# Kernel optimization log

Measured on AMD Instinct MI355X. Metric: run time of the kernel, lower is better.

## Reference

```python
import jax, jax.numpy as jnp
import numpy as np

N_HEADS = 16

def setup_inputs() -> dict:
    key = jax.random.key(0)
    qkv = jax.random.normal(key, (4, 3072, 1024), dtype=jnp.float32)
    return {"qkv": qkv}

def reference(qkv):
    bs, width, length = qkv.shape
    ch = width // (3 * N_HEADS)
    qkv_h = qkv.reshape(bs * N_HEADS, 3 * ch, length)
    q, k, v = jnp.split(qkv_h, 3, axis=1)  # each [bs*H, ch, T]
    scale = 1.0 / jnp.sqrt(jnp.sqrt(jnp.asarray(ch, qkv.dtype)))
    # [bs*H, T, T] scores
    weight = jnp.einsum('bct,bcs->bts', q * scale, k * scale)
    weight = jax.nn.softmax(weight.astype(jnp.float32), axis=-1).astype(weight.dtype)
    a = jnp.einsum('bts,bcs->bct', weight, v)  # [bs*H, ch, T]
    return a.reshape(bs, -1, length)
```

## Files before the change

### kernel.cpp

```cpp
#include <hip/hip_runtime.h>
#include <hip/hip_bf16.h>


typedef __bf16 bf16_8 __attribute__((ext_vector_type(8)));
typedef __bf16 bf16_4 __attribute__((ext_vector_type(4)));
typedef float floatx4 __attribute__((ext_vector_type(4)));
typedef float floatx16 __attribute__((ext_vector_type(16)));

#define NTHREADS 512
#define STR 64
#define NSTEPS 16

#if __has_builtin(__builtin_amdgcn_exp2f)
#define EXP2(x) __builtin_amdgcn_exp2f(x)
#else
#define EXP2(x) exp2f(x)
#endif
#define QSCALE 0.18033688011112042f

#define LDS_BYTES 57344

#define ZERO16 (floatx16){0.f,0.f,0.f,0.f,0.f,0.f,0.f,0.f,0.f,0.f,0.f,0.f,0.f,0.f,0.f,0.f}

__device__ __forceinline__ int kap(int row) { return ((row >> 1) + (row >> 4)) & 7; }
__device__ __forceinline__ int sigma_row(int s) {
    return (s & 0x33) | ((s & 4) << 1) | ((s & 8) >> 1);
}

__device__ __forceinline__ unsigned pk_bf16(float a, float b) {
    unsigned r;
    asm("v_cvt_pk_bf16_f32 %0, %1, %2" : "=v"(r) : "v"(a), "v"(b));
    return r;
}

union U8 { unsigned u[4]; bf16_8 v; };

__device__ __forceinline__ void write_k(__bf16* kn, const float4* r, int si, int sG) {
    #pragma unroll
    for (int rr = 0; rr < 4; ++rr) {
        int srow = si * 4 + rr;
        int m = sigma_row(srow);
        bf16_4 w;
        w[0] = (__bf16)((const float*)&r[0])[rr];
        w[1] = (__bf16)((const float*)&r[1])[rr];
        w[2] = (__bf16)((const float*)&r[2])[rr];
        w[3] = (__bf16)((const float*)&r[3])[rr];
        *(bf16_4*)&kn[m * STR + ((sG ^ (kap(m) << 1)) << 2)] = w;
    }
}
__device__ __forceinline__ void write_v(__bf16* vn, const float4* r, int si, int c0) {
    #pragma unroll
    for (int jj = 0; jj < 4; ++jj) {
        int c = c0 + jj;
        bf16_4 w;
        w[0] = (__bf16)r[jj].x; w[1] = (__bf16)r[jj].y;
        w[2] = (__bf16)r[jj].z; w[3] = (__bf16)r[jj].w;
        *(bf16_4*)&vn[c * STR + ((si ^ (kap(c) << 1)) << 2)] = w;
    }
}

__global__ __launch_bounds__(NTHREADS, 4)
void attn_kernel(const float* __restrict__ qkv, float* __restrict__ out) {
    __shared__ char smem[LDS_BYTES];
    __bf16* q_s = (__bf16*)smem;
    __bf16* k0  = (__bf16*)(smem + 16384);
    __bf16* k1  = (__bf16*)(smem + 24576);
    __bf16* v0  = (__bf16*)(smem + 32768);
    __bf16* v1  = (__bf16*)(smem + 40960);
    __bf16* v2  = (__bf16*)(smem + 49152);

    const int tid  = threadIdx.x;
    const int wave = tid >> 6;
    const int lane = tid & 63;
    const int hv   = lane >> 5;
    const int l31  = lane & 31;
    const int g    = wave >> 1;
    const int sh   = wave & 1;

    const int bx = blockIdx.x;
    const int bh = bx & 63;
    const int t0 = (bx >> 6) << 7;

    const float* qg = qkv + (size_t)bh * 196608;
    const float* kg = qg + 65536;
    const float* vg = qg + 131072;

    const int sv = tid >> 8;
    const int st = tid & 255;
    const int si = st & 15;
    const int sG = st >> 4;
    const int c0 = sG << 2;
    const float* gsrc = sv ? vg : kg;

    {
        const int cG = tid >> 5;
        const int ti = tid & 31;
        float4 q4[4];
        #pragma unroll
        for (int jj = 0; jj < 4; ++jj)
            q4[jj] = *(const float4*)(qg + (cG * 4 + jj) * 1024 + t0 + ti * 4);
        #pragma unroll
        for (int rr = 0; rr < 4; ++rr) {
            int trow = ti * 4 + rr;
            bf16_4 w;
            w[0] = (__bf16)(((const float*)&q4[0])[rr] * QSCALE);
            w[1] = (__bf16)(((const float*)&q4[1])[rr] * QSCALE);
            w[2] = (__bf16)(((const float*)&q4[2])[rr] * QSCALE);
            w[3] = (__bf16)(((const float*)&q4[3])[rr] * QSCALE);
            *(bf16_4*)&q_s[trow * STR + ((cG ^ (kap(trow) << 1)) << 2)] = w;
        }
    }
    {
        float4 r4[4];
        #pragma unroll
        for (int jj = 0; jj < 4; ++jj)
            r4[jj] = *(const float4*)(gsrc + (c0 + jj) * 1024 + si * 4);
        if (!sv) write_k(k0, r4, si, sG);
        else     write_v(v0, r4, si, c0);
    }
    __syncthreads();

    bf16_8 qf[4];
    {
        int row = g * 32 + l31;
        int x = kap(row);
        #pragma unroll
        for (int kc = 0; kc < 4; ++kc)
            qf[kc] = *(const bf16_8*)&q_s[row * STR + ((((kc << 1) | hv) ^ x) << 3)];
    }

    floatx16 O0 = ZERO16, O1 = ZERO16;
    float l = 0.f;
    bf16_8 pfp0, pfp1;
    int vprev = 2, vcur = 0, vnext = 1;

    const int krow = sh * 32 + l31;
    const int kx   = kap(krow);
    const int vx0  = kap(l31);
    const int vx1  = kap(32 + l31);

    for (int is = 0; is < NSTEPS; ++is) {
        const __bf16* kb = (is & 1) ? k1 : k0;

        float4 pr[4];
        if (is < NSTEPS - 1) {
            const int s0n = (is + 1) * 64;
            #pragma unroll
            for (int jj = 0; jj < 4; ++jj)
                pr[jj] = *(const float4*)(gsrc + (c0 + jj) * 1024 + s0n + si * 4);
        }

        floatx16 St = ZERO16;
        #pragma unroll
        for (int kc = 0; kc < 4; ++kc) {
            bf16_8 kf = *(const bf16_8*)&kb[krow * STR + ((((kc << 1) | hv) ^ kx) << 3)];
            St = __builtin_amdgcn_mfma_f32_32x32x16_bf16(kf, qf[kc], St, 0, 0, 0);
        }

        U8 w0, w1;
        #pragma unroll
        for (int d = 0; d < 4; ++d) {
            float pa = EXP2(St[2 * d]);
            float pb = EXP2(St[2 * d + 1]);
            float pc = EXP2(St[8 + 2 * d]);
            float pd = EXP2(St[8 + 2 * d + 1]);
            l += (pa + pb) + (pc + pd);
            w0.u[d] = pk_bf16(pa, pb);
            w1.u[d] = pk_bf16(pc, pd);
        }
        bf16_8 pfn0 = w0.v, pfn1 = w1.v;

        if (is > 0) {
            const __bf16* vp = (vprev == 0) ? v0 : ((vprev == 1) ? v1 : v2);
            {
                int vrow = l31;
                bf16_8 vfa = *(const bf16_8*)&vp[vrow * STR + ((((sh << 2) | hv) ^ vx0) << 3)];
                O0 = __builtin_amdgcn_mfma_f32_32x32x16_bf16(vfa, pfp0, O0, 0, 0, 0);
                bf16_8 vfb = *(const bf16_8*)&vp[vrow * STR + ((((sh << 2) | 2 | hv) ^ vx0) << 3)];
                O0 = __builtin_amdgcn_mfma_f32_32x32x16_bf16(vfb, pfp1, O0, 0, 0, 0);
            }
            {
                int vrow = 32 + l31;
                bf16_8 vfa = *(const bf16_8*)&vp[vrow * STR + ((((sh << 2) | hv) ^ vx1) << 3)];
                O1 = __builtin_amdgcn_mfma_f32_32x32x16_bf16(vfa, pfp0, O1, 0, 0, 0);
                bf16_8 vfb = *(const bf16_8*)&vp[vrow * STR + ((((sh << 2) | 2 | hv) ^ vx1) << 3)];
                O1 = __builtin_amdgcn_mfma_f32_32x32x16_bf16(vfb, pfp1, O1, 0, 0, 0);
            }
        }
        pfp0 = pfn0; pfp1 = pfn1;

        if (is < NSTEPS - 1) {
            if (!sv) {
                __bf16* kn = (is & 1) ? k0 : k1;
                write_k(kn, pr, si, sG);
            } else {
                __bf16* vn = (vnext == 0) ? v0 : ((vnext == 1) ? v1 : v2);
                write_v(vn, pr, si, c0);
            }
            __syncthreads();
        }
        vprev = vcur; vcur = vnext; vnext = (vnext == 2) ? 0 : vnext + 1;
    }

    {
        const __bf16* vp = (vprev == 0) ? v0 : ((vprev == 1) ? v1 : v2);
        {
            int vrow = l31;
            bf16_8 vfa = *(const bf16_8*)&vp[vrow * STR + ((((sh << 2) | hv) ^ vx0) << 3)];
            O0 = __builtin_amdgcn_mfma_f32_32x32x16_bf16(vfa, pfp0, O0, 0, 0, 0);
            bf16_8 vfb = *(const bf16_8*)&vp[vrow * STR + ((((sh << 2) | 2 | hv) ^ vx0) << 3)];
            O0 = __builtin_amdgcn_mfma_f32_32x32x16_bf16(vfb, pfp1, O0, 0, 0, 0);
        }
        {
            int vrow = 32 + l31;
            bf16_8 vfa = *(const bf16_8*)&vp[vrow * STR + ((((sh << 2) | hv) ^ vx1) << 3)];
            O1 = __builtin_amdgcn_mfma_f32_32x32x16_bf16(vfa, pfp0, O1, 0, 0, 0);
            bf16_8 vfb = *(const bf16_8*)&vp[vrow * STR + ((((sh << 2) | 2 | hv) ^ vx1) << 3)];
            O1 = __builtin_amdgcn_mfma_f32_32x32x16_bf16(vfb, pfp1, O1, 0, 0, 0);
        }
    }

    l += __shfl_xor(l, 32);

    __syncthreads();
    float* xo = (float*)smem;
    float* xl = (float*)(smem + 40960);
    if (sh == 1) {
        float* b = xo + g * 2048;
        #pragma unroll
        for (int rq = 0; rq < 4; ++rq) {
            floatx4 a0 = {O0[4 * rq], O0[4 * rq + 1], O0[4 * rq + 2], O0[4 * rq + 3]};
            *(floatx4*)&b[(rq * 64 + lane) * 4] = a0;
            floatx4 a1 = {O1[4 * rq], O1[4 * rq + 1], O1[4 * rq + 2], O1[4 * rq + 3]};
            *(floatx4*)&b[((4 + rq) * 64 + lane) * 4] = a1;
        }
        xl[g * 64 + lane] = l;
    }
    __syncthreads();
    if (sh == 0) {
        const float* b = xo + g * 2048;
        const float lt = l + xl[g * 64 + lane];
        const float linv = 1.0f / lt;
        float* og = out + (size_t)bh * 65536 + t0 + g * 32;
        #pragma unroll
        for (int rq = 0; rq < 4; ++rq) {
            floatx4 a0 = *(const floatx4*)&b[(rq * 64 + lane) * 4];
            floatx4 a1 = *(const floatx4*)&b[((4 + rq) * 64 + lane) * 4];
            #pragma unroll
            for (int j = 0; j < 4; ++j) {
                int cl = j + 8 * rq + 4 * hv;
                og[cl * 1024 + l31] = (O0[4 * rq + j] + a0[j]) * linv;
                og[(32 + cl) * 1024 + l31] = (O1[4 * rq + j] + a1[j]) * linv;
            }
        }
    }
}

extern "C" void kernel_launch(void* const* d_in, const int* in_sizes, int n_in,
                              void* d_out, int out_size, void* d_ws, size_t ws_size,
                              hipStream_t stream) {
    const float* qkv = (const float*)d_in[0];
    float* out = (float*)d_out;
    attn_kernel<<<dim3(512), dim3(NTHREADS), 0, stream>>>(qkv, out);
}
```

Before: 105.5 us.

## Double query tile per block to 256 rows and load Q straight to registers

Each block now runs 1024 threads and covers 256 query rows, so the grid shrinks from 512 to 256 blocks. Every K/V tile staged in LDS is reused by twice as many query waves, which halves redundant global K/V traffic. Q fragments are built directly in registers from global memory instead of going through an LDS staging buffer. The epilogue cross-wave reduction is split into two phases so it fits in the smaller LDS. The trade-off is one large block per CU with no overlap between blocks, an extra sync in the epilogue, and tighter register limits from the launch bounds.

```diff
diff --git a/kernel.cpp b/kernel.cpp
--- a/kernel.cpp
+++ b/kernel.cpp
@@ -7,7 +7,7 @@
 typedef float floatx4 __attribute__((ext_vector_type(4)));
 typedef float floatx16 __attribute__((ext_vector_type(16)));
 
-#define NTHREADS 512
+#define NTHREADS 1024
 #define STR 64
 #define NSTEPS 16
 
@@ -18,7 +18,7 @@
 #endif
 #define QSCALE 0.18033688011112042f
 
-#define LDS_BYTES 57344
+#define LDS_BYTES 43008
 
 #define ZERO16 (floatx16){0.f,0.f,0.f,0.f,0.f,0.f,0.f,0.f,0.f,0.f,0.f,0.f,0.f,0.f,0.f,0.f}
 
@@ -62,12 +62,11 @@
 __global__ __launch_bounds__(NTHREADS, 4)
 void attn_kernel(const float* __restrict__ qkv, float* __restrict__ out) {
     __shared__ char smem[LDS_BYTES];
-    __bf16* q_s = (__bf16*)smem;
-    __bf16* k0  = (__bf16*)(smem + 16384);
-    __bf16* k1  = (__bf16*)(smem + 24576);
+    __bf16* k0  = (__bf16*)smem;
+    __bf16* k1  = (__bf16*)(smem + 8192);
+    __bf16* v1  = (__bf16*)(smem + 16384);
+    __bf16* v2  = (__bf16*)(smem + 24576);
     __bf16* v0  = (__bf16*)(smem + 32768);
-    __bf16* v1  = (__bf16*)(smem + 40960);
-    __bf16* v2  = (__bf16*)(smem + 49152);
 
     const int tid  = threadIdx.x;
     const int wave = tid >> 6;
@@ -79,55 +78,44 @@
 
     const int bx = blockIdx.x;
     const int bh = bx & 63;
-    const int t0 = (bx >> 6) << 7;
+    const int t0 = (bx >> 6) << 8;
 
     const float* qg = qkv + (size_t)bh * 196608;
     const float* kg = qg + 65536;
     const float* vg = qg + 131072;
 
-    const int sv = tid >> 8;
+    const int stager = (tid < 512);
     const int st = tid & 255;
     const int si = st & 15;
     const int sG = st >> 4;
     const int c0 = sG << 2;
-    const float* gsrc = sv ? vg : kg;
-
+    const float* gsrc = (tid < 256) ? kg : vg;
+
+    bf16_8 qf[4];
     {
-        const int cG = tid >> 5;
-        const int ti = tid & 31;
-        float4 q4[4];
-        #pragma unroll
-        for (int jj = 0; jj < 4; ++jj)
-            q4[jj] = *(const float4*)(qg + (cG * 4 + jj) * 1024 + t0 + ti * 4);
-        #pragma unroll
-        for (int rr = 0; rr < 4; ++rr) {
-            int trow = ti * 4 + rr;
-            bf16_4 w;
-            w[0] = (__bf16)(((const float*)&q4[0])[rr] * QSCALE);
-            w[1] = (__bf16)(((const float*)&q4[1])[rr] * QSCALE);
-            w[2] = (__bf16)(((const float*)&q4[2])[rr] * QSCALE);
-            w[3] = (__bf16)(((const float*)&q4[3])[rr] * QSCALE);
-            *(bf16_4*)&q_s[trow * STR + ((cG ^ (kap(trow) << 1)) << 2)] = w;
-        }
-    }
-    {
+        const int tq = t0 + g * 32 + l31;
+        #pragma unroll
+        for (int kc = 0; kc < 4; ++kc) {
+            U8 w;
+            #pragma unroll
+            for (int d = 0; d < 4; ++d) {
+                float f0 = qg[(16 * kc + 8 * hv + 2 * d) * 1024 + tq] * QSCALE;
+                float f1 = qg[(16 * kc + 8 * hv + 2 * d + 1) * 1024 + tq] * QSCALE;
+                w.u[d] = pk_bf16(f0, f1);
+            }
+            qf[kc] = w.v;
+        }
+    }
+
+    if (stager) {
         float4 r4[4];
         #pragma unroll
         for (int jj = 0; jj < 4; ++jj)
             r4[jj] = *(const float4*)(gsrc + (c0 + jj) * 1024 + si * 4);
-        if (!sv) write_k(k0, r4, si, sG);
-        else     write_v(v0, r4, si, c0);
-    }
-    __syncthreads();
-
-    bf16_8 qf[4];
-    {
-        int row = g * 32 + l31;
-        int x = kap(row);
-        #pragma unroll
-        for (int kc = 0; kc < 4; ++kc)
-            qf[kc] = *(const bf16_8*)&q_s[row * STR + ((((kc << 1) | hv) ^ x) << 3)];
-    }
+        if (tid < 256) write_k(k0, r4, si, sG);
+        else           write_v(v0, r4, si, c0);
+    }
+    __syncthreads();
 
     floatx16 O0 = ZERO16, O1 = ZERO16;
     float l = 0.f;
@@ -143,7 +131,7 @@
         const __bf16* kb = (is & 1) ? k1 : k0;
 
         float4 pr[4];
-        if (is < NSTEPS - 1) {
+        if (stager && is < NSTEPS - 1) {
             const int s0n = (is + 1) * 64;
             #pragma unroll
             for (int jj = 0; jj < 4; ++jj)
@@ -190,12 +178,14 @@
         pfp0 = pfn0; pfp1 = pfn1;
 
         if (is < NSTEPS - 1) {
-            if (!sv) {
-                __bf16* kn = (is & 1) ? k0 : k1;
-                write_k(kn, pr, si, sG);
-            } else {
-                __bf16* vn = (vnext == 0) ? v0 : ((vnext == 1) ? v1 : v2);
-                write_v(vn, pr, si, c0);
+            if (stager) {
+                if (tid < 256) {
+                    __bf16* kn = (is & 1) ? k0 : k1;
+                    write_k(kn, pr, si, sG);
+                } else {
+                    __bf16* vn = (vnext == 0) ? v0 : ((vnext == 1) ? v1 : v2);
+                    write_v(vn, pr, si, c0);
+                }
             }
             __syncthreads();
         }
@@ -225,31 +215,48 @@
     __syncthreads();
     float* xo = (float*)smem;
     float* xl = (float*)(smem + 40960);
+    float* b  = xo + g * 1024;
+
     if (sh == 1) {
-        float* b = xo + g * 2048;
         #pragma unroll
         for (int rq = 0; rq < 4; ++rq) {
             floatx4 a0 = {O0[4 * rq], O0[4 * rq + 1], O0[4 * rq + 2], O0[4 * rq + 3]};
             *(floatx4*)&b[(rq * 64 + lane) * 4] = a0;
-            floatx4 a1 = {O1[4 * rq], O1[4 * rq + 1], O1[4 * rq + 2], O1[4 * rq + 3]};
-            *(floatx4*)&b[((4 + rq) * 64 + lane) * 4] = a1;
         }
         xl[g * 64 + lane] = l;
     }
     __syncthreads();
+    float linv = 0.f;
+    float* og = out + (size_t)bh * 65536 + t0 + g * 32;
     if (sh == 0) {
-        const float* b = xo + g * 2048;
         const float lt = l + xl[g * 64 + lane];
-        const float linv = 1.0f / lt;
-        float* og = out + (size_t)bh * 65536 + t0 + g * 32;
+        linv = 1.0f / lt;
         #pragma unroll
         for (int rq = 0; rq < 4; ++rq) {
             floatx4 a0 = *(const floatx4*)&b[(rq * 64 + lane) * 4];
-            floatx4 a1 = *(const floatx4*)&b[((4 + rq) * 64 + lane) * 4];
             #pragma unroll
             for (int j = 0; j < 4; ++j) {
                 int cl = j + 8 * rq + 4 * hv;
                 og[cl * 1024 + l31] = (O0[4 * rq + j] + a0[j]) * linv;
+            }
+        }
+    }
+    __syncthreads();
+    if (sh == 1) {
+        #pragma unroll
+        for (int rq = 0; rq < 4; ++rq) {
+            floatx4 a1 = {O1[4 * rq], O1[4 * rq + 1], O1[4 * rq + 2], O1[4 * rq + 3]};
+            *(floatx4*)&b[(rq * 64 + lane) * 4] = a1;
+        }
+    }
+    __syncthreads();
+    if (sh == 0) {
+        #pragma unroll
+        for (int rq = 0; rq < 4; ++rq) {
+            floatx4 a1 = *(const floatx4*)&b[(rq * 64 + lane) * 4];
+            #pragma unroll
+            for (int j = 0; j < 4; ++j) {
+                int cl = j + 8 * rq + 4 * hv;
                 og[(32 + cl) * 1024 + l31] = (O1[4 * rq + j] + a1[j]) * linv;
             }
         }
@@ -261,5 +268,5 @@
                               hipStream_t stream) {
     const float* qkv = (const float*)d_in[0];
     float* out = (float*)d_out;
-    attn_kernel<<<dim3(512), dim3(NTHREADS), 0, stream>>>(qkv, out);
-}
+    attn_kernel<<<dim3(256), dim3(NTHREADS), 0, stream>>>(qkv, out);
+}
```

Result: slower. 120.2 us (+13.9%).

## Load Q fragments directly, prefetch K/V two steps ahead, add MFMA priority hints

Applied to the files above, without the earlier changes.

Removes the Q staging buffer in LDS: each lane gathers its Q fragment straight from global memory, scales it and packs it to bf16, which cuts LDS from 56 KB to 40 KB. K/V global prefetch now runs two tiles ahead with a register rotation, giving loads more time to land. MFMA sections are wrapped in s_setprio, and bf16 conversions use packed v_cvt_pk_bf16_f32. The trade-off is strided scalar global loads for Q and higher register pressure from the extra prefetch buffer.

```diff
diff --git a/kernel.cpp b/kernel.cpp
--- a/kernel.cpp
+++ b/kernel.cpp
@@ -18,7 +18,7 @@
 #endif
 #define QSCALE 0.18033688011112042f
 
-#define LDS_BYTES 57344
+#define LDS_BYTES 40960
 
 #define ZERO16 (floatx16){0.f,0.f,0.f,0.f,0.f,0.f,0.f,0.f,0.f,0.f,0.f,0.f,0.f,0.f,0.f,0.f}
 
@@ -34,40 +34,38 @@
 }
 
 union U8 { unsigned u[4]; bf16_8 v; };
+union U4 { unsigned u[2]; bf16_4 v; };
 
 __device__ __forceinline__ void write_k(__bf16* kn, const float4* r, int si, int sG) {
     #pragma unroll
     for (int rr = 0; rr < 4; ++rr) {
         int srow = si * 4 + rr;
         int m = sigma_row(srow);
-        bf16_4 w;
-        w[0] = (__bf16)((const float*)&r[0])[rr];
-        w[1] = (__bf16)((const float*)&r[1])[rr];
-        w[2] = (__bf16)((const float*)&r[2])[rr];
-        w[3] = (__bf16)((const float*)&r[3])[rr];
-        *(bf16_4*)&kn[m * STR + ((sG ^ (kap(m) << 1)) << 2)] = w;
+        U4 w;
+        w.u[0] = pk_bf16(((const float*)&r[0])[rr], ((const float*)&r[1])[rr]);
+        w.u[1] = pk_bf16(((const float*)&r[2])[rr], ((const float*)&r[3])[rr]);
+        *(bf16_4*)&kn[m * STR + ((sG ^ (kap(m) << 1)) << 2)] = w.v;
     }
 }
 __device__ __forceinline__ void write_v(__bf16* vn, const float4* r, int si, int c0) {
     #pragma unroll
     for (int jj = 0; jj < 4; ++jj) {
         int c = c0 + jj;
-        bf16_4 w;
-        w[0] = (__bf16)r[jj].x; w[1] = (__bf16)r[jj].y;
-        w[2] = (__bf16)r[jj].z; w[3] = (__bf16)r[jj].w;
-        *(bf16_4*)&vn[c * STR + ((si ^ (kap(c) << 1)) << 2)] = w;
+        U4 w;
+        w.u[0] = pk_bf16(r[jj].x, r[jj].y);
+        w.u[1] = pk_bf16(r[jj].z, r[jj].w);
+        *(bf16_4*)&vn[c * STR + ((si ^ (kap(c) << 1)) << 2)] = w.v;
     }
 }
 
 __global__ __launch_bounds__(NTHREADS, 4)
 void attn_kernel(const float* __restrict__ qkv, float* __restrict__ out) {
     __shared__ char smem[LDS_BYTES];
-    __bf16* q_s = (__bf16*)smem;
-    __bf16* k0  = (__bf16*)(smem + 16384);
-    __bf16* k1  = (__bf16*)(smem + 24576);
-    __bf16* v0  = (__bf16*)(smem + 32768);
-    __bf16* v1  = (__bf16*)(smem + 40960);
-    __bf16* v2  = (__bf16*)(smem + 49152);
+    __bf16* k0  = (__bf16*)smem;
+    __bf16* k1  = (__bf16*)(smem + 8192);
+    __bf16* v0  = (__bf16*)(smem + 16384);
+    __bf16* v1  = (__bf16*)(smem + 24576);
+    __bf16* v2  = (__bf16*)(smem + 32768);
 
     const int tid  = threadIdx.x;
     const int wave = tid >> 6;
@@ -92,42 +90,35 @@
     const int c0 = sG << 2;
     const float* gsrc = sv ? vg : kg;
 
-    {
-        const int cG = tid >> 5;
-        const int ti = tid & 31;
-        float4 q4[4];
-        #pragma unroll
-        for (int jj = 0; jj < 4; ++jj)
-            q4[jj] = *(const float4*)(qg + (cG * 4 + jj) * 1024 + t0 + ti * 4);
-        #pragma unroll
-        for (int rr = 0; rr < 4; ++rr) {
-            int trow = ti * 4 + rr;
-            bf16_4 w;
-            w[0] = (__bf16)(((const float*)&q4[0])[rr] * QSCALE);
-            w[1] = (__bf16)(((const float*)&q4[1])[rr] * QSCALE);
-            w[2] = (__bf16)(((const float*)&q4[2])[rr] * QSCALE);
-            w[3] = (__bf16)(((const float*)&q4[3])[rr] * QSCALE);
-            *(bf16_4*)&q_s[trow * STR + ((cG ^ (kap(trow) << 1)) << 2)] = w;
-        }
-    }
-    {
-        float4 r4[4];
-        #pragma unroll
-        for (int jj = 0; jj < 4; ++jj)
-            r4[jj] = *(const float4*)(gsrc + (c0 + jj) * 1024 + si * 4);
-        if (!sv) write_k(k0, r4, si, sG);
-        else     write_v(v0, r4, si, c0);
-    }
-    __syncthreads();
+    float4 r4[4];
+    #pragma unroll
+    for (int jj = 0; jj < 4; ++jj)
+        r4[jj] = *(const float4*)(gsrc + (c0 + jj) * 1024 + si * 4);
 
     bf16_8 qf[4];
     {
-        int row = g * 32 + l31;
-        int x = kap(row);
-        #pragma unroll
-        for (int kc = 0; kc < 4; ++kc)
-            qf[kc] = *(const bf16_8*)&q_s[row * STR + ((((kc << 1) | hv) ^ x) << 3)];
-    }
+        const int tq = t0 + g * 32 + l31;
+        #pragma unroll
+        for (int kc = 0; kc < 4; ++kc) {
+            U8 w;
+            #pragma unroll
+            for (int d = 0; d < 4; ++d) {
+                float f0 = qg[(16 * kc + 8 * hv + 2 * d) * 1024 + tq] * QSCALE;
+                float f1 = qg[(16 * kc + 8 * hv + 2 * d + 1) * 1024 + tq] * QSCALE;
+                w.u[d] = pk_bf16(f0, f1);
+            }
+            qf[kc] = w.v;
+        }
+    }
+
+    float4 prA[4];
+    #pragma unroll
+    for (int jj = 0; jj < 4; ++jj)
+        prA[jj] = *(const float4*)(gsrc + (c0 + jj) * 1024 + 64 + si * 4);
+
+    if (!sv) write_k(k0, r4, si, sG);
+    else     write_v(v0, r4, si, c0);
+    __syncthreads();
 
     floatx16 O0 = ZERO16, O1 = ZERO16;
     float l = 0.f;
@@ -142,20 +133,22 @@
     for (int is = 0; is < NSTEPS; ++is) {
         const __bf16* kb = (is & 1) ? k1 : k0;
 
-        float4 pr[4];
-        if (is < NSTEPS - 1) {
-            const int s0n = (is + 1) * 64;
+        float4 prB[4];
+        if (is < NSTEPS - 2) {
+            const int s0n = (is + 2) * 64;
             #pragma unroll
             for (int jj = 0; jj < 4; ++jj)
-                pr[jj] = *(const float4*)(gsrc + (c0 + jj) * 1024 + s0n + si * 4);
+                prB[jj] = *(const float4*)(gsrc + (c0 + jj) * 1024 + s0n + si * 4);
         }
 
         floatx16 St = ZERO16;
+        __builtin_amdgcn_s_setprio(1);
         #pragma unroll
         for (int kc = 0; kc < 4; ++kc) {
             bf16_8 kf = *(const bf16_8*)&kb[krow * STR + ((((kc << 1) | hv) ^ kx) << 3)];
             St = __builtin_amdgcn_mfma_f32_32x32x16_bf16(kf, qf[kc], St, 0, 0, 0);
         }
+        __builtin_amdgcn_s_setprio(0);
 
         U8 w0, w1;
         #pragma unroll
@@ -172,6 +165,7 @@
 
         if (is > 0) {
             const __bf16* vp = (vprev == 0) ? v0 : ((vprev == 1) ? v1 : v2);
+            __builtin_amdgcn_s_setprio(1);
             {
                 int vrow = l31;
                 bf16_8 vfa = *(const bf16_8*)&vp[vrow * STR + ((((sh << 2) | hv) ^ vx0) << 3)];
@@ -186,19 +180,22 @@
                 bf16_8 vfb = *(const bf16_8*)&vp[vrow * STR + ((((sh << 2) | 2 | hv) ^ vx1) << 3)];
                 O1 = __builtin_amdgcn_mfma_f32_32x32x16_bf16(vfb, pfp1, O1, 0, 0, 0);
             }
+            __builtin_amdgcn_s_setprio(0);
         }
         pfp0 = pfn0; pfp1 = pfn1;
 
         if (is < NSTEPS - 1) {
             if (!sv) {
                 __bf16* kn = (is & 1) ? k0 : k1;
-                write_k(kn, pr, si, sG);
+                write_k(kn, prA, si, sG);
             } else {
                 __bf16* vn = (vnext == 0) ? v0 : ((vnext == 1) ? v1 : v2);
-                write_v(vn, pr, si, c0);
+                write_v(vn, prA, si, c0);
             }
             __syncthreads();
         }
+        #pragma unroll
+        for (int jj = 0; jj < 4; ++jj) prA[jj] = prB[jj];
         vprev = vcur; vcur = vnext; vnext = (vnext == 2) ? 0 : vnext + 1;
     }
 
@@ -224,7 +221,7 @@
 
     __syncthreads();
     float* xo = (float*)smem;
-    float* xl = (float*)(smem + 40960);
+    float* xl = (float*)(smem + 32768);
     if (sh == 1) {
         float* b = xo + g * 2048;
         #pragma unroll
```

New measurement: 126.1 us. 1.2x slower.
